# Kernel tuning notes

Hardware: AMD Instinct MI355X
Metric: run time of the kernel (lower is better)

Reference implementation:

```python
import jax, jax.numpy as jnp
import numpy as np

N_NODES = 50000
N_EDGES = 800000
IN_CH = 256
HID_CH = 128


def setup_inputs() -> dict:
    key = jax.random.key(0)
    k1, k2, k3, k4, k5 = jax.random.split(key, 5)
    x = jax.random.normal(k1, (N_NODES, IN_CH), dtype=jnp.float32)
    edge_index = jax.random.randint(k2, (2, N_EDGES), 0, N_NODES, dtype=jnp.int64)
    edge_weight = jax.random.uniform(k3, (N_EDGES,), dtype=jnp.float32)
    W = jax.random.normal(k4, (IN_CH, HID_CH), dtype=jnp.float32) * (1.0 / np.sqrt(IN_CH))
    b = jnp.zeros((HID_CH,), dtype=jnp.float32)
    alpha = jnp.full((HID_CH,), 0.25, dtype=jnp.float32)  # PReLU default init
    return {"x": x, "edge_index": edge_index, "edge_weight": edge_weight,
            "W": W, "b": b, "alpha": alpha}


def reference(x, edge_index, edge_weight, W, b, alpha):
    """GCNConv (with self-loops + symmetric normalization) followed by PReLU."""
    N = x.shape[0]
    row, col = edge_index[0], edge_index[1]
    # add self-loops with weight 1 (PyG gcn_norm default, add_self_loops=True)
    loop = jnp.arange(N, dtype=row.dtype)
    row = jnp.concatenate([row, loop])
    col = jnp.concatenate([col, loop])
    ew = jnp.concatenate([edge_weight, jnp.ones((N,), dtype=edge_weight.dtype)])
    # degree from edge weights, scattered at destination (col)
    deg = jax.ops.segment_sum(ew, col, num_segments=N)
    deg_inv_sqrt = jnp.where(deg > 0, jax.lax.rsqrt(deg), 0.0)
    norm = deg_inv_sqrt[row] * ew * deg_inv_sqrt[col]  # [E+N]
    # linear transform then gather-scale-scatter aggregation
    h = x @ W                               # [N, HID]
    msg = h[row] * norm[:, None]            # [E+N, HID]
    out = jax.ops.segment_sum(msg, col, num_segments=N) + b
    # PReLU with per-channel slope
    return jnp.where(out >= 0, out, alpha * out)
```

## Files before the change

### kernel.cpp

```cpp
#include <hip/hip_runtime.h>

#define NN 50000
#define NE 800000
#define KD 256
#define CD 128
#define NB 196
#define GEMM_BLOCKS 782
#define HIST_BLOCKS 3125

typedef __attribute__((ext_vector_type(8))) short short8;
typedef __attribute__((ext_vector_type(4))) float floatx4;

__device__ inline unsigned short f2bf(float f) {
    unsigned u = __float_as_uint(f);
    unsigned r = (u + 0x7FFFu + ((u >> 16) & 1u)) >> 16;
    return (unsigned short)r;
}
__device__ inline float bf2f_lo(unsigned u) { return __uint_as_float(u << 16); }
__device__ inline float bf2f_hi(unsigned u) { return __uint_as_float(u & 0xFFFF0000u); }

__global__ __launch_bounds__(256) void fused_gemm_hist(
        const float* __restrict__ x, const unsigned short* __restrict__ Wt,
        unsigned short* __restrict__ hb,
        const int* __restrict__ col, const float* __restrict__ ew,
        unsigned long long* __restrict__ packedAll, unsigned short* __restrict__ rank) {
    __shared__ unsigned short As[64][40];
    __shared__ unsigned short Bs[128][40];

    if (blockIdx.x >= GEMM_BLOCKS) {
        const int hblk = blockIdx.x - GEMM_BLOCKS;
        int e = hblk * 256 + threadIdx.x;
        if (e < NE) {
            unsigned long long* packed = packedAll + (size_t)(hblk & 3) * NN;
            unsigned long long p = (1ull << 40)
                                 + (unsigned long long)(ew[e] * 4294967296.0f);
            unsigned long long old = atomicAdd(&packed[col[e]], p);
            rank[e] = (unsigned short)(old >> 40);
        }
        return;
    }

    const int tid  = threadIdx.x;
    const int wave = tid >> 6;
    const int lane = tid & 63;
    const int row0 = blockIdx.x * 64;
    const int m0   = wave * 16;
    const int lr   = lane & 15;
    const int quad = lane >> 4;

    const int ar = tid >> 2;
    const int aq = tid & 3;
    const int bn = tid >> 1;
    const int bh = (tid & 1) * 16;

    floatx4 acc[8];
#pragma unroll
    for (int nt = 0; nt < 8; nt++) acc[nt] = (floatx4){0.f, 0.f, 0.f, 0.f};

    for (int kt = 0; kt < 8; kt++) {
        const int k0 = kt * 32;
        union { short8 v; unsigned short u[8]; } av;
        const int gr = row0 + ar;
        if (gr < NN) {
            const float* xp = x + (size_t)gr * KD + k0 + aq * 8;
            float4 f0 = *(const float4*)xp;
            float4 f1 = *(const float4*)(xp + 4);
            av.u[0] = f2bf(f0.x); av.u[1] = f2bf(f0.y);
            av.u[2] = f2bf(f0.z); av.u[3] = f2bf(f0.w);
            av.u[4] = f2bf(f1.x); av.u[5] = f2bf(f1.y);
            av.u[6] = f2bf(f1.z); av.u[7] = f2bf(f1.w);
        } else {
            av.v = (short8){0,0,0,0,0,0,0,0};
        }
        *(short8*)&As[ar][aq * 8] = av.v;
        const unsigned short* wp = Wt + (size_t)bn * KD + k0 + bh;
        *(short8*)&Bs[bn][bh]     = *(const short8*)wp;
        *(short8*)&Bs[bn][bh + 8] = *(const short8*)(wp + 8);
        __syncthreads();
        short8 af = *(const short8*)&As[m0 + lr][quad * 8];
#pragma unroll
        for (int nt = 0; nt < 8; nt++) {
            short8 bfr = *(const short8*)&Bs[nt * 16 + lr][quad * 8];
            acc[nt] = __builtin_amdgcn_mfma_f32_16x16x32_bf16(af, bfr, acc[nt], 0, 0, 0);
        }
        __syncthreads();
    }

#pragma unroll
    for (int i = 0; i < 4; i++) {
        const int grow = row0 + m0 + quad * 4 + i;
        if (grow < NN) {
            unsigned short* hp = hb + (size_t)grow * CD + lr;
#pragma unroll
            for (int nt = 0; nt < 8; nt++)
                hp[nt * 16] = f2bf(acc[nt][i]);
        }
    }
}

__global__ __launch_bounds__(256) void scan_blocks(const unsigned long long* __restrict__ packedAll,
                                                   int* __restrict__ local,
                                                   int* __restrict__ partials) {
    __shared__ int sm[256];
    const int t = threadIdx.x;
    const int g = blockIdx.x * 256 + t;
    int v = 0;
    if (g < NN) {
#pragma unroll
        for (int c = 0; c < 4; c++)
            v += (int)(packedAll[(size_t)c * NN + g] >> 40);
    }
    sm[t] = v;
    __syncthreads();
#pragma unroll
    for (int off = 1; off < 256; off <<= 1) {
        int u = (t >= off) ? sm[t - off] : 0;
        __syncthreads();
        sm[t] += u;
        __syncthreads();
    }
    local[g] = sm[t] - v;
    if (t == 255) partials[blockIdx.x] = sm[t];
}

__global__ __launch_bounds__(256) void scan_apply(const int* __restrict__ local,
                                                  const int* __restrict__ partials,
                                                  const unsigned long long* __restrict__ packedAll,
                                                  int* __restrict__ start,
                                                  int4* __restrict__ base4,
                                                  float* __restrict__ dinv) {
    __shared__ int sm[256];
    const int t = threadIdx.x;
    const int b = blockIdx.x;
    sm[t] = (t < b) ? partials[t] : 0;
    __syncthreads();
#pragma unroll
    for (int off = 128; off > 0; off >>= 1) {
        if (t < off) sm[t] += sm[t + off];
        __syncthreads();
    }
    const int base = sm[0];
    const int g = b * 256 + t;
    if (g < NN) {
        int cc[4];
        unsigned long long lowsum = 0;
#pragma unroll
        for (int c = 0; c < 4; c++) {
            unsigned long long p = packedAll[(size_t)c * NN + g];
            cc[c] = (int)(p >> 40);
            lowsum += p & ((1ull << 40) - 1);
        }
        const int s = local[g] + base;
        start[g] = s;
        base4[g] = make_int4(s, s + cc[0], s + cc[0] + cc[1], s + cc[0] + cc[1] + cc[2]);
        float degs = (float)lowsum * (1.0f / 4294967296.0f);
        dinv[g] = rsqrtf(1.0f + degs);
    }
    if (g == 0) start[NN] = NE;
}

__global__ __launch_bounds__(256) void meta_write(const int* __restrict__ row,
                                                  const int* __restrict__ col,
                                                  const float* __restrict__ ew,
                                                  const unsigned short* __restrict__ rank,
                                                  const int4* __restrict__ base4,
                                                  const float* __restrict__ dinv,
                                                  unsigned* __restrict__ meta) {
    int e = blockIdx.x * 256 + threadIdx.x;
    if (e >= NE) return;
    const int copy = blockIdx.x & 3;
    int c = col[e];
    int r = row[e];
    int4 b4 = base4[c];
    int base = (copy == 0) ? b4.x : (copy == 1) ? b4.y : (copy == 2) ? b4.z : b4.w;
    int pos = base + rank[e];
    unsigned short wbf = f2bf(dinv[r] * ew[e]);
    meta[pos] = ((unsigned)wbf << 16) | (unsigned)r;
}

__global__ __launch_bounds__(256) void w_transpose(const float* __restrict__ W,
                                                   unsigned short* __restrict__ Wt) {
    __shared__ unsigned short t[32][33];
    const int bk = blockIdx.x * 32;
    const int bn = blockIdx.y * 32;
    const int tx = threadIdx.x & 31;
    const int ty = threadIdx.x >> 5;
#pragma unroll
    for (int i = 0; i < 32; i += 8)
        t[ty + i][tx] = f2bf(W[(size_t)(bk + ty + i) * CD + bn + tx]);
    __syncthreads();
#pragma unroll
    for (int i = 0; i < 32; i += 8)
        Wt[(size_t)(bn + ty + i) * KD + bk + tx] = t[tx][ty + i];
}

__global__ __launch_bounds__(256) void aggregate(const int* __restrict__ start,
                                                 const unsigned* __restrict__ meta,
                                                 const unsigned short* __restrict__ hb,
                                                 const float* __restrict__ dinv,
                                                 const float* __restrict__ bias,
                                                 const float* __restrict__ alpha,
                                                 float* __restrict__ out) {
    int n = blockIdx.x * 4 + (threadIdx.x >> 6);
    if (n >= NN) return;
    n = __builtin_amdgcn_readfirstlane(n);
    const int lane = threadIdx.x & 63;
    const int s = __builtin_amdgcn_readfirstlane(start[n]);
    const int e = __builtin_amdgcn_readfirstlane(start[n + 1]);

    float A0[8], A1[8];
#pragma unroll
    for (int j = 0; j < 8; j++) { A0[j] = 0.f; A1[j] = 0.f; }

    int i = s;
    for (; i + 8 <= e; i += 8) {
        unsigned m[8], u[8];
#pragma unroll
        for (int j = 0; j < 8; j++) m[j] = meta[i + j];
#pragma unroll
        for (int j = 0; j < 8; j++)
            u[j] = *(const unsigned*)(hb + (size_t)(m[j] & 0xFFFFu) * CD + lane * 2);
#pragma unroll
        for (int j = 0; j < 8; j++) {
            float w = __uint_as_float(m[j] & 0xFFFF0000u);
            A0[j] = fmaf(w, bf2f_lo(u[j]), A0[j]);
            A1[j] = fmaf(w, bf2f_hi(u[j]), A1[j]);
        }
    }
    for (; i < e; i++) {
        unsigned m = meta[i];
        unsigned u = *(const unsigned*)(hb + (size_t)(m & 0xFFFFu) * CD + lane * 2);
        float w = __uint_as_float(m & 0xFFFF0000u);
        A0[0] = fmaf(w, bf2f_lo(u), A0[0]);
        A1[0] = fmaf(w, bf2f_hi(u), A1[0]);
    }
#pragma unroll
    for (int j = 1; j < 8; j++) { A0[0] += A0[j]; A1[0] += A1[j]; }

    const float dc = dinv[n];
    unsigned us = *(const unsigned*)(hb + (size_t)n * CD + lane * 2);
    const int ch = lane * 2;
    float o0 = dc * A0[0] + dc * dc * bf2f_lo(us) + bias[ch];
    float o1 = dc * A1[0] + dc * dc * bf2f_hi(us) + bias[ch + 1];
    o0 = o0 >= 0.f ? o0 : alpha[ch] * o0;
    o1 = o1 >= 0.f ? o1 : alpha[ch + 1] * o1;
    *(float2*)(out + (size_t)n * CD + ch) = make_float2(o0, o1);
}

extern "C" void kernel_launch(void* const* d_in, const int* in_sizes, int n_in,
                              void* d_out, int out_size, void* d_ws, size_t ws_size,
                              hipStream_t stream) {
    const float* x     = (const float*)d_in[0];
    const int*   eidx  = (const int*)d_in[1];
    const float* ew    = (const float*)d_in[2];
    const float* Wm    = (const float*)d_in[3];
    const float* bias  = (const float*)d_in[4];
    const float* alpha = (const float*)d_in[5];
    const int* row = eidx;
    const int* col = eidx + NE;

    float* out = (float*)d_out;

    char* ws = (char*)d_ws;
    unsigned long long* packedAll = (unsigned long long*)(ws);
    int*   start    = (int*)(ws + 1600000);
    int*   local    = (int*)(ws + 1800016);
    int*   partials = (int*)(ws + 2000720);
    float* dinv     = (float*)(ws + 2001504);
    unsigned short* rank = (unsigned short*)(ws + 2201504);
    int4*  base4    = (int4*)(ws + 3801504);
    unsigned* meta  = (unsigned*)(ws + 4601504);
    unsigned short* Wt = (unsigned short*)(ws + 7801504);
    unsigned short* hb = (unsigned short*)(ws + 7867040);

    hipMemsetAsync(ws, 0, 1600000, stream);
    w_transpose   <<<dim3(8, 4), 256, 0, stream>>>(Wm, Wt);
    fused_gemm_hist<<<GEMM_BLOCKS + HIST_BLOCKS, 256, 0, stream>>>(
                        x, Wt, hb, col, ew, packedAll, rank);
    scan_blocks   <<<NB, 256, 0, stream>>>(packedAll, local, partials);
    scan_apply    <<<NB, 256, 0, stream>>>(local, partials, packedAll, start, base4, dinv);
    meta_write    <<<(NE + 255) / 256, 256, 0, stream>>>(row, col, ew, rank, base4, dinv, meta);
    aggregate     <<<(NN + 3) / 4, 256, 0, stream>>>(start, meta, hb, dinv, bias, alpha, out);
}
```

Measured before the change: 203.4 us.

## Regroup kernels: fuse GEMM with meta write, 32-bit packed histogram, prefetch GEMM loads

Moves the GEMM out of the histogram kernel and fuses it with the meta-write pass. The memset and W transpose are folded into one prep kernel, which cuts one launch. The degree/count histogram now packs into 32-bit atomics (8-bit count, 24-bit fixed-point weight) instead of 64-bit, which halves the atomic and scan traffic. The GEMM now register-prefetches the next k-tile of x and W. The narrower packing lowers degree precision to 2^-18 and limits per-copy counts to 255, which could overflow for high-degree nodes.

Result: slower. 209.7 us (+3.1%).

```diff
diff --git a/kernel.cpp b/kernel.cpp
--- a/kernel.cpp
+++ b/kernel.cpp
@@ -19,86 +19,46 @@
 __device__ inline float bf2f_lo(unsigned u) { return __uint_as_float(u << 16); }
 __device__ inline float bf2f_hi(unsigned u) { return __uint_as_float(u & 0xFFFF0000u); }
 
-__global__ __launch_bounds__(256) void fused_gemm_hist(
-        const float* __restrict__ x, const unsigned short* __restrict__ Wt,
-        unsigned short* __restrict__ hb,
-        const int* __restrict__ col, const float* __restrict__ ew,
-        unsigned long long* __restrict__ packedAll, unsigned short* __restrict__ rank) {
-    __shared__ unsigned short As[64][40];
-    __shared__ unsigned short Bs[128][40];
-
-    if (blockIdx.x >= GEMM_BLOCKS) {
-        const int hblk = blockIdx.x - GEMM_BLOCKS;
-        int e = hblk * 256 + threadIdx.x;
-        if (e < NE) {
-            unsigned long long* packed = packedAll + (size_t)(hblk & 3) * NN;
-            unsigned long long p = (1ull << 40)
-                                 + (unsigned long long)(ew[e] * 4294967296.0f);
-            unsigned long long old = atomicAdd(&packed[col[e]], p);
-            rank[e] = (unsigned short)(old >> 40);
+__global__ __launch_bounds__(256) void prep(const float* __restrict__ W,
+                                            unsigned short* __restrict__ Wt,
+                                            unsigned* __restrict__ packedAll) {
+    __shared__ unsigned short t[32][33];
+    if (blockIdx.x < NB) {
+        const int g = blockIdx.x * 256 + threadIdx.x;
+        if (g < NN) {
+#pragma unroll
+            for (int c = 0; c < 4; c++) packedAll[(size_t)c * NN + g] = 0u;
         }
         return;
     }
-
-    const int tid  = threadIdx.x;
-    const int wave = tid >> 6;
-    const int lane = tid & 63;
-    const int row0 = blockIdx.x * 64;
-    const int m0   = wave * 16;
-    const int lr   = lane & 15;
-    const int quad = lane >> 4;
-
-    const int ar = tid >> 2;
-    const int aq = tid & 3;
-    const int bn = tid >> 1;
-    const int bh = (tid & 1) * 16;
-
-    floatx4 acc[8];
-#pragma unroll
-    for (int nt = 0; nt < 8; nt++) acc[nt] = (floatx4){0.f, 0.f, 0.f, 0.f};
-
-    for (int kt = 0; kt < 8; kt++) {
-        const int k0 = kt * 32;
-        union { short8 v; unsigned short u[8]; } av;
-        const int gr = row0 + ar;
-        if (gr < NN) {
-            const float* xp = x + (size_t)gr * KD + k0 + aq * 8;
-            float4 f0 = *(const float4*)xp;
-            float4 f1 = *(const float4*)(xp + 4);
-            av.u[0] = f2bf(f0.x); av.u[1] = f2bf(f0.y);
-            av.u[2] = f2bf(f0.z); av.u[3] = f2bf(f0.w);
-            av.u[4] = f2bf(f1.x); av.u[5] = f2bf(f1.y);
-            av.u[6] = f2bf(f1.z); av.u[7] = f2bf(f1.w);
-        } else {
-            av.v = (short8){0,0,0,0,0,0,0,0};
-        }
-        *(short8*)&As[ar][aq * 8] = av.v;
-        const unsigned short* wp = Wt + (size_t)bn * KD + k0 + bh;
-        *(short8*)&Bs[bn][bh]     = *(const short8*)wp;
-        *(short8*)&Bs[bn][bh + 8] = *(const short8*)(wp + 8);
-        __syncthreads();
-        short8 af = *(const short8*)&As[m0 + lr][quad * 8];
-#pragma unroll
-        for (int nt = 0; nt < 8; nt++) {
-            short8 bfr = *(const short8*)&Bs[nt * 16 + lr][quad * 8];
-            acc[nt] = __builtin_amdgcn_mfma_f32_16x16x32_bf16(af, bfr, acc[nt], 0, 0, 0);
-        }
-        __syncthreads();
-    }
-
-#pragma unroll
-    for (int i = 0; i < 4; i++) {
-        const int grow = row0 + m0 + quad * 4 + i;
-        if (grow < NN) {
-            unsigned short* hp = hb + (size_t)grow * CD + lr;
-#pragma unroll
-            for (int nt = 0; nt < 8; nt++)
-                hp[nt * 16] = f2bf(acc[nt][i]);
-        }
-    }
-}
-
-__global__ __launch_bounds__(256) void scan_blocks(const unsigned long long* __restrict__ packedAll,
+    const int b2 = blockIdx.x - NB;
+    const int bk = (b2 & 7) * 32;
+    const int bn = (b2 >> 3) * 32;
+    const int tx = threadIdx.x & 31;
+    const int ty = threadIdx.x >> 5;
+#pragma unroll
+    for (int i = 0; i < 32; i += 8)
+        t[ty + i][tx] = f2bf(W[(size_t)(bk + ty + i) * CD + bn + tx]);
+    __syncthreads();
+#pragma unroll
+    for (int i = 0; i < 32; i += 8)
+        Wt[(size_t)(bn + ty + i) * KD + bk + tx] = t[tx][ty + i];
+}
+
+__global__ __launch_bounds__(256) void hist(const int* __restrict__ col,
+                                            const float* __restrict__ ew,
+                                            unsigned* __restrict__ packedAll,
+                                            unsigned short* __restrict__ rank) {
+    const int e = blockIdx.x * 256 + threadIdx.x;
+    if (e < NE) {
+        unsigned* packed = packedAll + (size_t)(blockIdx.x & 3) * NN;
+        unsigned p = (1u << 24) + (unsigned)(ew[e] * 262144.0f);
+        unsigned old = atomicAdd(&packed[col[e]], p);
+        rank[e] = (unsigned short)(old >> 24);
+    }
+}
+
+__global__ __launch_bounds__(256) void scan_blocks(const unsigned* __restrict__ packedAll,
                                                    int* __restrict__ local,
                                                    int* __restrict__ partials) {
     __shared__ int sm[256];
@@ -108,7 +68,7 @@
     if (g < NN) {
 #pragma unroll
         for (int c = 0; c < 4; c++)
-            v += (int)(packedAll[(size_t)c * NN + g] >> 40);
+            v += (int)(packedAll[(size_t)c * NN + g] >> 24);
     }
     sm[t] = v;
     __syncthreads();
@@ -125,7 +85,7 @@
 
 __global__ __launch_bounds__(256) void scan_apply(const int* __restrict__ local,
                                                   const int* __restrict__ partials,
-                                                  const unsigned long long* __restrict__ packedAll,
+                                                  const unsigned* __restrict__ packedAll,
                                                   int* __restrict__ start,
                                                   int4* __restrict__ base4,
                                                   float* __restrict__ dinv) {
@@ -143,55 +103,117 @@
     const int g = b * 256 + t;
     if (g < NN) {
         int cc[4];
-        unsigned long long lowsum = 0;
+        unsigned lowsum = 0;
 #pragma unroll
         for (int c = 0; c < 4; c++) {
-            unsigned long long p = packedAll[(size_t)c * NN + g];
-            cc[c] = (int)(p >> 40);
-            lowsum += p & ((1ull << 40) - 1);
+            unsigned p = packedAll[(size_t)c * NN + g];
+            cc[c] = (int)(p >> 24);
+            lowsum += p & 0xFFFFFFu;
         }
         const int s = local[g] + base;
         start[g] = s;
         base4[g] = make_int4(s, s + cc[0], s + cc[0] + cc[1], s + cc[0] + cc[1] + cc[2]);
-        float degs = (float)lowsum * (1.0f / 4294967296.0f);
+        float degs = (float)lowsum * (1.0f / 262144.0f);
         dinv[g] = rsqrtf(1.0f + degs);
     }
     if (g == 0) start[NN] = NE;
 }
 
-__global__ __launch_bounds__(256) void meta_write(const int* __restrict__ row,
-                                                  const int* __restrict__ col,
-                                                  const float* __restrict__ ew,
-                                                  const unsigned short* __restrict__ rank,
-                                                  const int4* __restrict__ base4,
-                                                  const float* __restrict__ dinv,
-                                                  unsigned* __restrict__ meta) {
-    int e = blockIdx.x * 256 + threadIdx.x;
-    if (e >= NE) return;
-    const int copy = blockIdx.x & 3;
-    int c = col[e];
-    int r = row[e];
-    int4 b4 = base4[c];
-    int base = (copy == 0) ? b4.x : (copy == 1) ? b4.y : (copy == 2) ? b4.z : b4.w;
-    int pos = base + rank[e];
-    unsigned short wbf = f2bf(dinv[r] * ew[e]);
-    meta[pos] = ((unsigned)wbf << 16) | (unsigned)r;
-}
-
-__global__ __launch_bounds__(256) void w_transpose(const float* __restrict__ W,
-                                                   unsigned short* __restrict__ Wt) {
-    __shared__ unsigned short t[32][33];
-    const int bk = blockIdx.x * 32;
-    const int bn = blockIdx.y * 32;
-    const int tx = threadIdx.x & 31;
-    const int ty = threadIdx.x >> 5;
-#pragma unroll
-    for (int i = 0; i < 32; i += 8)
-        t[ty + i][tx] = f2bf(W[(size_t)(bk + ty + i) * CD + bn + tx]);
-    __syncthreads();
-#pragma unroll
-    for (int i = 0; i < 32; i += 8)
-        Wt[(size_t)(bn + ty + i) * KD + bk + tx] = t[tx][ty + i];
+__global__ __launch_bounds__(256) void gemm_meta(
+        const float* __restrict__ x, const unsigned short* __restrict__ Wt,
+        unsigned short* __restrict__ hb,
+        const int* __restrict__ row, const int* __restrict__ col,
+        const float* __restrict__ ew, const unsigned short* __restrict__ rank,
+        const int4* __restrict__ base4, const float* __restrict__ dinv,
+        unsigned* __restrict__ meta) {
+    __shared__ unsigned short As[64][40];
+    __shared__ unsigned short Bs[128][40];
+
+    if (blockIdx.x >= GEMM_BLOCKS) {
+        const int mblk = blockIdx.x - GEMM_BLOCKS;
+        const int e = mblk * 256 + threadIdx.x;
+        if (e < NE) {
+            const int copy = mblk & 3;
+            int c = col[e];
+            int r = row[e];
+            int4 b4 = base4[c];
+            int base = (copy == 0) ? b4.x : (copy == 1) ? b4.y : (copy == 2) ? b4.z : b4.w;
+            int pos = base + rank[e];
+            unsigned short wbf = f2bf(dinv[r] * ew[e]);
+            meta[pos] = ((unsigned)wbf << 16) | (unsigned)r;
+        }
+        return;
+    }
+
+    const int tid  = threadIdx.x;
+    const int wave = tid >> 6;
+    const int lane = tid & 63;
+    const int row0 = blockIdx.x * 64;
+    const int m0   = wave * 16;
+    const int lr   = lane & 15;
+    const int quad = lane >> 4;
+
+    const int ar = tid >> 2;
+    const int aq = tid & 3;
+    const int bn = tid >> 1;
+    const int bh = (tid & 1) * 16;
+
+    const int gr = row0 + ar;
+    const bool arow_ok = gr < NN;
+    const float* xbase = x + (size_t)gr * KD + aq * 8;
+    const unsigned short* wbase = Wt + (size_t)bn * KD + bh;
+
+    floatx4 acc[8];
+#pragma unroll
+    for (int nt = 0; nt < 8; nt++) acc[nt] = (floatx4){0.f, 0.f, 0.f, 0.f};
+
+    float4 f0 = {0.f, 0.f, 0.f, 0.f}, f1 = {0.f, 0.f, 0.f, 0.f};
+    short8 wv0, wv1;
+    if (arow_ok) { f0 = *(const float4*)xbase; f1 = *(const float4*)(xbase + 4); }
+    wv0 = *(const short8*)wbase;
+    wv1 = *(const short8*)(wbase + 8);
+
+#pragma unroll
+    for (int kt = 0; kt < 8; kt++) {
+        union { short8 v; unsigned short u[8]; } av;
+        if (arow_ok) {
+            av.u[0] = f2bf(f0.x); av.u[1] = f2bf(f0.y);
+            av.u[2] = f2bf(f0.z); av.u[3] = f2bf(f0.w);
+            av.u[4] = f2bf(f1.x); av.u[5] = f2bf(f1.y);
+            av.u[6] = f2bf(f1.z); av.u[7] = f2bf(f1.w);
+        } else {
+            av.v = (short8){0,0,0,0,0,0,0,0};
+        }
+        *(short8*)&As[ar][aq * 8] = av.v;
+        *(short8*)&Bs[bn][bh]     = wv0;
+        *(short8*)&Bs[bn][bh + 8] = wv1;
+        __syncthreads();
+        if (kt < 7) {
+            const float* xp = xbase + (kt + 1) * 32;
+            if (arow_ok) { f0 = *(const float4*)xp; f1 = *(const float4*)(xp + 4); }
+            const unsigned short* wp = wbase + (kt + 1) * 32;
+            wv0 = *(const short8*)wp;
+            wv1 = *(const short8*)(wp + 8);
+        }
+        short8 af = *(const short8*)&As[m0 + lr][quad * 8];
+#pragma unroll
+        for (int nt = 0; nt < 8; nt++) {
+            short8 bfr = *(const short8*)&Bs[nt * 16 + lr][quad * 8];
+            acc[nt] = __builtin_amdgcn_mfma_f32_16x16x32_bf16(af, bfr, acc[nt], 0, 0, 0);
+        }
+        __syncthreads();
+    }
+
+#pragma unroll
+    for (int i = 0; i < 4; i++) {
+        const int grow = row0 + m0 + quad * 4 + i;
+        if (grow < NN) {
+            unsigned short* hp = hb + (size_t)grow * CD + lr;
+#pragma unroll
+            for (int nt = 0; nt < 8; nt++)
+                hp[nt * 16] = f2bf(acc[nt][i]);
+        }
+    }
 }
 
 __global__ __launch_bounds__(256) void aggregate(const int* __restrict__ start,
@@ -262,23 +284,22 @@
     float* out = (float*)d_out;
 
     char* ws = (char*)d_ws;
-    unsigned long long* packedAll = (unsigned long long*)(ws);
-    int*   start    = (int*)(ws + 1600000);
-    int*   local    = (int*)(ws + 1800016);
-    int*   partials = (int*)(ws + 2000720);
-    float* dinv     = (float*)(ws + 2001504);
-    unsigned short* rank = (unsigned short*)(ws + 2201504);
-    int4*  base4    = (int4*)(ws + 3801504);
-    unsigned* meta  = (unsigned*)(ws + 4601504);
-    unsigned short* Wt = (unsigned short*)(ws + 7801504);
-    unsigned short* hb = (unsigned short*)(ws + 7867040);
-
-    hipMemsetAsync(ws, 0, 1600000, stream);
-    w_transpose   <<<dim3(8, 4), 256, 0, stream>>>(Wm, Wt);
-    fused_gemm_hist<<<GEMM_BLOCKS + HIST_BLOCKS, 256, 0, stream>>>(
-                        x, Wt, hb, col, ew, packedAll, rank);
-    scan_blocks   <<<NB, 256, 0, stream>>>(packedAll, local, partials);
-    scan_apply    <<<NB, 256, 0, stream>>>(local, partials, packedAll, start, base4, dinv);
-    meta_write    <<<(NE + 255) / 256, 256, 0, stream>>>(row, col, ew, rank, base4, dinv, meta);
-    aggregate     <<<(NN + 3) / 4, 256, 0, stream>>>(start, meta, hb, dinv, bias, alpha, out);
-}
+    unsigned* packedAll = (unsigned*)(ws);
+    int*   start    = (int*)(ws + 800000);
+    int*   local    = (int*)(ws + 1000064);
+    int*   partials = (int*)(ws + 1200768);
+    float* dinv     = (float*)(ws + 1201552);
+    unsigned short* rank = (unsigned short*)(ws + 1401552);
+    int4*  base4    = (int4*)(ws + 3001552);
+    unsigned* meta  = (unsigned*)(ws + 3801552);
+    unsigned short* Wt = (unsigned short*)(ws + 7001552);
+    unsigned short* hb = (unsigned short*)(ws + 7067088);
+
+    prep       <<<NB + 32, 256, 0, stream>>>(Wm, Wt, packedAll);
+    hist       <<<HIST_BLOCKS, 256, 0, stream>>>(col, ew, packedAll, rank);
+    scan_blocks<<<NB, 256, 0, stream>>>(packedAll, local, partials);
+    scan_apply <<<NB, 256, 0, stream>>>(local, partials, packedAll, start, base4, dinv);
+    gemm_meta  <<<GEMM_BLOCKS + HIST_BLOCKS, 256, 0, stream>>>(
+                    x, Wt, hb, row, col, ew, rank, base4, dinv, meta);
+    aggregate  <<<(NN + 3) / 4, 256, 0, stream>>>(start, meta, hb, dinv, bias, alpha, out);
+}
```
